# Kernel optimization log

Measured on AMD Instinct MI355X. Metric: run time of the kernel, lower is better.

The kernel has to match this reference:

```python
import jax, jax.numpy as jnp
import numpy as np

TEMPERATURE = 0.1
EPS = 1e-12  # matches F.normalize eps clamp


def setup_inputs() -> dict:
    key = jax.random.key(0)
    k1, k2 = jax.random.split(key)
    B, D = 4096, 1024
    z1 = jax.random.normal(k1, (B, D), dtype=jnp.float32)
    z2 = jax.random.normal(k2, (B, D), dtype=jnp.float32)
    return {"z1": z1, "z2": z2}


def reference(z1, z2):
    B = z1.shape[0]
    # L2-normalize rows (F.normalize dim=1, eps clamp)
    n1 = z1 / jnp.maximum(jnp.linalg.norm(z1, axis=1, keepdims=True), EPS)
    n2 = z2 / jnp.maximum(jnp.linalg.norm(z2, axis=1, keepdims=True), EPS)
    reps = jnp.concatenate([n1, n2], axis=0)  # [2B, D]
    # Rows are unit-norm, so cosine similarity == dot product -> one GEMM
    sim = (reps @ reps.T) / TEMPERATURE  # [2B, 2B]
    # positives: diag offsets +B and -B
    pos = jnp.concatenate([jnp.diagonal(sim, B), jnp.diagonal(sim, -B)])  # [2B]
    # logits row i = [pos_i, sim[i, j != i]]. logsumexp over that set =
    # logaddexp(pos_i, logsumexp over the row with the main diagonal removed).
    eye = jnp.eye(2 * B, dtype=bool)
    masked = jnp.where(eye, -jnp.inf, sim)
    lse_neg = jax.scipy.special.logsumexp(masked, axis=1)  # [2B]
    lse = jnp.logaddexp(pos, lse_neg)
    # CrossEntropyLoss with labels==0 -> mean(lse - logit_0) = mean(lse - pos)
    return jnp.mean(lse - pos)
```

## Files before the change

### kernel.cpp

```cpp
#include <hip/hip_runtime.h>

#define D_DIM 1024
#define B_HALF 4096
#define NROWS 8192
#define INV_TEMP 10.0f
#define NT 32
#define NKT 16

typedef __bf16 bf16x8 __attribute__((ext_vector_type(8)));
typedef float floatx4 __attribute__((ext_vector_type(4)));

#define MFMA16 __builtin_amdgcn_mfma_f32_16x16x32_bf16

__device__ __forceinline__ unsigned short f32_to_bf16(float f) {
    union { float f; unsigned u; } v; v.f = f;
    unsigned r = 0x7FFFu + ((v.u >> 16) & 1u);
    return (unsigned short)((v.u + r) >> 16);
}

__global__ __launch_bounds__(256) void normalize_kernel(
    const float* __restrict__ z1, const float* __restrict__ z2,
    unsigned short* __restrict__ R)
{
    const int row = blockIdx.x;
    const int tid = threadIdx.x;
    const float* src = (row < B_HALF) ? (z1 + (size_t)row * D_DIM)
                                      : (z2 + (size_t)(row - B_HALF) * D_DIM);
    float4 v = ((const float4*)src)[tid];
    float ss = v.x * v.x + v.y * v.y + v.z * v.z + v.w * v.w;
    #pragma unroll
    for (int off = 32; off > 0; off >>= 1) ss += __shfl_down(ss, off);
    __shared__ float wsum[4];
    if ((tid & 63) == 0) wsum[tid >> 6] = ss;
    __syncthreads();
    float tot = wsum[0] + wsum[1] + wsum[2] + wsum[3];
    float scale = 1.0f / fmaxf(sqrtf(tot), 1e-12f);
    ushort4 o;
    o.x = f32_to_bf16(v.x * scale);
    o.y = f32_to_bf16(v.y * scale);
    o.z = f32_to_bf16(v.z * scale);
    o.w = f32_to_bf16(v.w * scale);
    ((ushort4*)(R + (size_t)row * D_DIM))[tid] = o;
}

__global__ __launch_bounds__(512, 2) void gemm_lse_kernel(
    const unsigned short* __restrict__ R,
    float* __restrict__ partial, float* __restrict__ pos)
{
    __shared__ unsigned short lds[2][2][256 * 64];

    int t = blockIdx.x;
    int rt = 0;
    while (t >= NT - rt) { t -= NT - rt; ++rt; }
    const int ct = rt + t;
    const bool isDiag = (rt == ct);

    const int tid = threadIdx.x;
    const int wave = tid >> 6, lane = tid & 63;
    const int wm = wave >> 2, wn = wave & 3;
    const int row0 = rt * 256, col0 = ct * 256;
    const int lm = lane & 15, lq = lane >> 4;

    const unsigned short* __restrict__ gA = R + (size_t)row0 * D_DIM;
    const unsigned short* __restrict__ gB = R + (size_t)col0 * D_DIM;

    const int sRow  = lane >> 3;
    const int sSlot = (lane & 7) ^ sRow;
    const int aOff = (wm * 128 + lm) * 64;
    const int bOff = (wn * 64 + lm) * 64;
    const int sk0 = ((0 + lq) ^ (lm & 7)) * 8;
    const int sk1 = ((4 + lq) ^ (lm & 7)) * 8;

    floatx4 acc[8][4] = {};

#define STAGE_A(dstbuf, kk) \
    { _Pragma("unroll") \
      for (int i = 0; i < 4; ++i) \
        __builtin_amdgcn_global_load_lds( \
          (const __attribute__((address_space(1))) unsigned int*)(gA + (size_t)(i * 64 + wave * 8 + sRow) * D_DIM + (kk) + sSlot * 8), \
          (__attribute__((address_space(3))) unsigned int*)(&lds[dstbuf][0][(i * 64 + wave * 8) * 64]), \
          16, 0, 0); }

#define STAGE_B(dstbuf, kk) \
    { _Pragma("unroll") \
      for (int i = 0; i < 4; ++i) \
        __builtin_amdgcn_global_load_lds( \
          (const __attribute__((address_space(1))) unsigned int*)(gB + (size_t)(i * 64 + wave * 8 + sRow) * D_DIM + (kk) + sSlot * 8), \
          (__attribute__((address_space(3))) unsigned int*)(&lds[dstbuf][1][(i * 64 + wave * 8) * 64]), \
          16, 0, 0); }

    STAGE_A(0, 0)
    STAGE_B(0, 0)
    asm volatile("s_waitcnt vmcnt(0)" ::: "memory");
    __builtin_amdgcn_s_barrier();

    bf16x8 a[4][2];
    bf16x8 b[2][2][2];

    for (int kt = 0; kt < NKT; ++kt) {
        const int buf = kt & 1;
        const unsigned short* As = &lds[buf][0][0];
        const unsigned short* Bs = &lds[buf][1][0];
        const int kn = (kt + 1) * 64;
        const bool more = (kt + 1 < NKT);

        if (more) STAGE_A(buf ^ 1, kn)
        #pragma unroll
        for (int mi = 0; mi < 4; ++mi) {
            a[mi][0] = *(const bf16x8*)(As + aOff + mi * 1024 + sk0);
            a[mi][1] = *(const bf16x8*)(As + aOff + mi * 1024 + sk1);
        }
        #pragma unroll
        for (int ni = 0; ni < 2; ++ni) {
            b[0][ni][0] = *(const bf16x8*)(Bs + bOff + ni * 1024 + sk0);
            b[0][ni][1] = *(const bf16x8*)(Bs + bOff + ni * 1024 + sk1);
        }
        __builtin_amdgcn_s_barrier();
        __builtin_amdgcn_s_setprio(1);
        #pragma unroll
        for (int mi = 0; mi < 4; ++mi)
            #pragma unroll
            for (int ni = 0; ni < 2; ++ni) {
                acc[mi][ni] = MFMA16(a[mi][0], b[0][ni][0], acc[mi][ni], 0, 0, 0);
                acc[mi][ni] = MFMA16(a[mi][1], b[0][ni][1], acc[mi][ni], 0, 0, 0);
            }
        __builtin_amdgcn_s_setprio(0);
        __builtin_amdgcn_s_barrier();

        if (more) STAGE_B(buf ^ 1, kn)
        #pragma unroll
        for (int ni = 0; ni < 2; ++ni) {
            b[1][ni][0] = *(const bf16x8*)(Bs + bOff + (2 + ni) * 1024 + sk0);
            b[1][ni][1] = *(const bf16x8*)(Bs + bOff + (2 + ni) * 1024 + sk1);
        }
        __builtin_amdgcn_s_barrier();
        __builtin_amdgcn_s_setprio(1);
        #pragma unroll
        for (int mi = 0; mi < 4; ++mi)
            #pragma unroll
            for (int ni = 0; ni < 2; ++ni) {
                acc[mi][2 + ni] = MFMA16(a[mi][0], b[1][ni][0], acc[mi][2 + ni], 0, 0, 0);
                acc[mi][2 + ni] = MFMA16(a[mi][1], b[1][ni][1], acc[mi][2 + ni], 0, 0, 0);
            }
        __builtin_amdgcn_s_setprio(0);
        __builtin_amdgcn_s_barrier();

        #pragma unroll
        for (int mi = 0; mi < 4; ++mi) {
            a[mi][0] = *(const bf16x8*)(As + aOff + (4 + mi) * 1024 + sk0);
            a[mi][1] = *(const bf16x8*)(As + aOff + (4 + mi) * 1024 + sk1);
        }
        __builtin_amdgcn_s_barrier();
        __builtin_amdgcn_s_setprio(1);
        #pragma unroll
        for (int mi = 0; mi < 4; ++mi)
            #pragma unroll
            for (int ni = 0; ni < 2; ++ni) {
                acc[4 + mi][ni] = MFMA16(a[mi][0], b[0][ni][0], acc[4 + mi][ni], 0, 0, 0);
                acc[4 + mi][ni] = MFMA16(a[mi][1], b[0][ni][1], acc[4 + mi][ni], 0, 0, 0);
            }
        __builtin_amdgcn_s_setprio(0);
        __builtin_amdgcn_s_barrier();

        __builtin_amdgcn_s_setprio(1);
        #pragma unroll
        for (int mi = 0; mi < 4; ++mi)
            #pragma unroll
            for (int ni = 0; ni < 2; ++ni) {
                acc[4 + mi][2 + ni] = MFMA16(a[mi][0], b[1][ni][0], acc[4 + mi][2 + ni], 0, 0, 0);
                acc[4 + mi][2 + ni] = MFMA16(a[mi][1], b[1][ni][1], acc[4 + mi][2 + ni], 0, 0, 0);
            }
        __builtin_amdgcn_s_setprio(0);
        asm volatile("s_waitcnt vmcnt(0)" ::: "memory");
        __builtin_amdgcn_s_barrier();
        asm volatile("" ::: "memory");
    }

    float* rowsum = (float*)&lds[0][0][0];
    float* colsum = rowsum + 4 * 256;

    float ecol[4] = {0.0f, 0.0f, 0.0f, 0.0f};
    #pragma unroll
    for (int mi = 0; mi < 8; ++mi) {
        #pragma unroll
        for (int reg = 0; reg < 4; ++reg) {
            const int gr = row0 + wm * 128 + mi * 16 + lq * 4 + reg;
            float esum = 0.0f;
            #pragma unroll
            for (int ni = 0; ni < 4; ++ni) {
                const int gc = col0 + wn * 64 + ni * 16 + lm;
                float s = acc[mi][ni][reg] * INV_TEMP;
                if (gc == gr + B_HALF) { pos[gr] = s; pos[gc] = s; }
                float e = (gc == gr) ? 0.0f : __expf(s);
                esum += e;
                ecol[ni] += e;
            }
            esum += __shfl_xor(esum, 1);
            esum += __shfl_xor(esum, 2);
            esum += __shfl_xor(esum, 4);
            esum += __shfl_xor(esum, 8);
            if (lm == 0) rowsum[wn * 256 + wm * 128 + mi * 16 + lq * 4 + reg] = esum;
        }
    }
    #pragma unroll
    for (int ni = 0; ni < 4; ++ni) {
        ecol[ni] += __shfl_xor(ecol[ni], 16);
        ecol[ni] += __shfl_xor(ecol[ni], 32);
    }
    if (lq == 0 && !isDiag) {
        #pragma unroll
        for (int ni = 0; ni < 4; ++ni)
            colsum[wm * 256 + wn * 64 + ni * 16 + lm] = ecol[ni];
    }
    __syncthreads();
    if (tid < 256) {
        float rs = rowsum[0 * 256 + tid] + rowsum[1 * 256 + tid]
                 + rowsum[2 * 256 + tid] + rowsum[3 * 256 + tid];
        partial[(size_t)(row0 + tid) * NT + ct] = rs;
        if (!isDiag) {
            float cs = colsum[0 * 256 + tid] + colsum[1 * 256 + tid];
            partial[(size_t)(col0 + tid) * NT + rt] = cs;
        }
    }
}

__global__ __launch_bounds__(256) void finalize_kernel(
    const float* __restrict__ partial, const float* __restrict__ pos,
    float* __restrict__ out)
{
    const int r = blockIdx.x * 256 + threadIdx.x;
    const float4* p = (const float4*)(partial + (size_t)r * NT);
    float S = 0.0f;
    #pragma unroll
    for (int i = 0; i < 8; ++i) { float4 v = p[i]; S += (v.x + v.y) + (v.z + v.w); }
    const float po = pos[r];
    float contrib = log1pf(S * __expf(-po));
    #pragma unroll
    for (int off = 32; off > 0; off >>= 1) contrib += __shfl_down(contrib, off);
    __shared__ float wsum[4];
    if ((threadIdx.x & 63) == 0) wsum[threadIdx.x >> 6] = contrib;
    __syncthreads();
    if (threadIdx.x == 0)
        atomicAdd(out, (wsum[0] + wsum[1] + wsum[2] + wsum[3]) * (1.0f / 8192.0f));
}

extern "C" void kernel_launch(void* const* d_in, const int* in_sizes, int n_in,
                              void* d_out, int out_size, void* d_ws, size_t ws_size,
                              hipStream_t stream)
{
    const float* z1 = (const float*)d_in[0];
    const float* z2 = (const float*)d_in[1];
    float* out = (float*)d_out;
    char* ws = (char*)d_ws;
    unsigned short* R = (unsigned short*)ws;
    float* partial = (float*)(ws + (size_t)16 * 1024 * 1024);
    float* pos     = (float*)(ws + (size_t)18 * 1024 * 1024);

    hipMemsetAsync(d_out, 0, sizeof(float), stream);
    normalize_kernel<<<NROWS, 256, 0, stream>>>(z1, z2, R);
    gemm_lse_kernel<<<528, 512, 0, stream>>>(R, partial, pos);
    finalize_kernel<<<32, 256, 0, stream>>>(partial, pos, out);
}
```

Baseline: 181.9 us.

## Halve GEMM K-tile to 32 and simplify main loop to single MFMA phase

Shrinks the K tile from 64 to 32, which halves LDS per buffer and doubles the loop trip count. The four-phase interleaved loop, with its staged A/B prefetch and several barriers, becomes one phase: load all A/B fragments, issue 32 MFMAs, then wait and barrier once. The swizzle and staging layout are redone for 32-wide rows. The smaller LDS footprint could allow more resident blocks and the loop has fewer barriers, but each iteration now has less work to hide global-load latency behind.

```diff
diff --git a/kernel.cpp b/kernel.cpp
--- a/kernel.cpp
+++ b/kernel.cpp
@@ -5,7 +5,7 @@
 #define NROWS 8192
 #define INV_TEMP 10.0f
 #define NT 32
-#define NKT 16
+#define NKT 32
 
 typedef __bf16 bf16x8 __attribute__((ext_vector_type(8)));
 typedef float floatx4 __attribute__((ext_vector_type(4)));
@@ -47,7 +47,7 @@
     const unsigned short* __restrict__ R,
     float* __restrict__ partial, float* __restrict__ pos)
 {
-    __shared__ unsigned short lds[2][2][256 * 64];
+    __shared__ unsigned short lds[2][2][256 * 32];
 
     int t = blockIdx.x;
     int rt = 0;
@@ -64,116 +64,56 @@
     const unsigned short* __restrict__ gA = R + (size_t)row0 * D_DIM;
     const unsigned short* __restrict__ gB = R + (size_t)col0 * D_DIM;
 
-    const int sRow  = lane >> 3;
-    const int sSlot = (lane & 7) ^ sRow;
-    const int aOff = (wm * 128 + lm) * 64;
-    const int bOff = (wn * 64 + lm) * 64;
-    const int sk0 = ((0 + lq) ^ (lm & 7)) * 8;
-    const int sk1 = ((4 + lq) ^ (lm & 7)) * 8;
+    const int sRow = lane >> 2;
+    const int sCol = (lane & 3) ^ ((sRow >> 1) & 3);
+    const int sk = ((lq ^ ((lm >> 1) & 3)) * 8);
+    const int aBase = (wm * 128 + lm) * 32 + sk;
+    const int bBase = (wn * 64 + lm) * 32 + sk;
 
     floatx4 acc[8][4] = {};
 
-#define STAGE_A(dstbuf, kk) \
+#define STAGE(dstbuf, kk) \
     { _Pragma("unroll") \
-      for (int i = 0; i < 4; ++i) \
+      for (int i = 0; i < 2; ++i) { \
         __builtin_amdgcn_global_load_lds( \
-          (const __attribute__((address_space(1))) unsigned int*)(gA + (size_t)(i * 64 + wave * 8 + sRow) * D_DIM + (kk) + sSlot * 8), \
-          (__attribute__((address_space(3))) unsigned int*)(&lds[dstbuf][0][(i * 64 + wave * 8) * 64]), \
-          16, 0, 0); }
-
-#define STAGE_B(dstbuf, kk) \
-    { _Pragma("unroll") \
-      for (int i = 0; i < 4; ++i) \
+          (const __attribute__((address_space(1))) unsigned int*)(gA + (size_t)(wave * 32 + i * 16 + sRow) * D_DIM + (kk) + sCol * 8), \
+          (__attribute__((address_space(3))) unsigned int*)(&lds[dstbuf][0][(wave * 32 + i * 16) * 32]), \
+          16, 0, 0); \
         __builtin_amdgcn_global_load_lds( \
-          (const __attribute__((address_space(1))) unsigned int*)(gB + (size_t)(i * 64 + wave * 8 + sRow) * D_DIM + (kk) + sSlot * 8), \
-          (__attribute__((address_space(3))) unsigned int*)(&lds[dstbuf][1][(i * 64 + wave * 8) * 64]), \
-          16, 0, 0); }
-
-    STAGE_A(0, 0)
-    STAGE_B(0, 0)
+          (const __attribute__((address_space(1))) unsigned int*)(gB + (size_t)(wave * 32 + i * 16 + sRow) * D_DIM + (kk) + sCol * 8), \
+          (__attribute__((address_space(3))) unsigned int*)(&lds[dstbuf][1][(wave * 32 + i * 16) * 32]), \
+          16, 0, 0); \
+      } }
+
+    STAGE(0, 0)
     asm volatile("s_waitcnt vmcnt(0)" ::: "memory");
     __builtin_amdgcn_s_barrier();
-
-    bf16x8 a[4][2];
-    bf16x8 b[2][2][2];
 
     for (int kt = 0; kt < NKT; ++kt) {
         const int buf = kt & 1;
         const unsigned short* As = &lds[buf][0][0];
         const unsigned short* Bs = &lds[buf][1][0];
-        const int kn = (kt + 1) * 64;
-        const bool more = (kt + 1 < NKT);
-
-        if (more) STAGE_A(buf ^ 1, kn)
-        #pragma unroll
-        for (int mi = 0; mi < 4; ++mi) {
-            a[mi][0] = *(const bf16x8*)(As + aOff + mi * 1024 + sk0);
-            a[mi][1] = *(const bf16x8*)(As + aOff + mi * 1024 + sk1);
-        }
-        #pragma unroll
-        for (int ni = 0; ni < 2; ++ni) {
-            b[0][ni][0] = *(const bf16x8*)(Bs + bOff + ni * 1024 + sk0);
-            b[0][ni][1] = *(const bf16x8*)(Bs + bOff + ni * 1024 + sk1);
-        }
-        __builtin_amdgcn_s_barrier();
+
+        if (kt + 1 < NKT) STAGE(buf ^ 1, (kt + 1) * 32)
+
+        bf16x8 af[8], bf[4];
+        #pragma unroll
+        for (int mi = 0; mi < 8; ++mi)
+            af[mi] = *(const bf16x8*)(As + aBase + mi * 512);
+        #pragma unroll
+        for (int ni = 0; ni < 4; ++ni)
+            bf[ni] = *(const bf16x8*)(Bs + bBase + ni * 512);
+
         __builtin_amdgcn_s_setprio(1);
         #pragma unroll
-        for (int mi = 0; mi < 4; ++mi)
+        for (int mi = 0; mi < 8; ++mi)
             #pragma unroll
-            for (int ni = 0; ni < 2; ++ni) {
-                acc[mi][ni] = MFMA16(a[mi][0], b[0][ni][0], acc[mi][ni], 0, 0, 0);
-                acc[mi][ni] = MFMA16(a[mi][1], b[0][ni][1], acc[mi][ni], 0, 0, 0);
-            }
+            for (int ni = 0; ni < 4; ++ni)
+                acc[mi][ni] = MFMA16(af[mi], bf[ni], acc[mi][ni], 0, 0, 0);
         __builtin_amdgcn_s_setprio(0);
-        __builtin_amdgcn_s_barrier();
-
-        if (more) STAGE_B(buf ^ 1, kn)
-        #pragma unroll
-        for (int ni = 0; ni < 2; ++ni) {
-            b[1][ni][0] = *(const bf16x8*)(Bs + bOff + (2 + ni) * 1024 + sk0);
-            b[1][ni][1] = *(const bf16x8*)(Bs + bOff + (2 + ni) * 1024 + sk1);
-        }
-        __builtin_amdgcn_s_barrier();
-        __builtin_amdgcn_s_setprio(1);
-        #pragma unroll
-        for (int mi = 0; mi < 4; ++mi)
-            #pragma unroll
-            for (int ni = 0; ni < 2; ++ni) {
-                acc[mi][2 + ni] = MFMA16(a[mi][0], b[1][ni][0], acc[mi][2 + ni], 0, 0, 0);
-                acc[mi][2 + ni] = MFMA16(a[mi][1], b[1][ni][1], acc[mi][2 + ni], 0, 0, 0);
-            }
-        __builtin_amdgcn_s_setprio(0);
-        __builtin_amdgcn_s_barrier();
-
-        #pragma unroll
-        for (int mi = 0; mi < 4; ++mi) {
-            a[mi][0] = *(const bf16x8*)(As + aOff + (4 + mi) * 1024 + sk0);
-            a[mi][1] = *(const bf16x8*)(As + aOff + (4 + mi) * 1024 + sk1);
-        }
-        __builtin_amdgcn_s_barrier();
-        __builtin_amdgcn_s_setprio(1);
-        #pragma unroll
-        for (int mi = 0; mi < 4; ++mi)
-            #pragma unroll
-            for (int ni = 0; ni < 2; ++ni) {
-                acc[4 + mi][ni] = MFMA16(a[mi][0], b[0][ni][0], acc[4 + mi][ni], 0, 0, 0);
-                acc[4 + mi][ni] = MFMA16(a[mi][1], b[0][ni][1], acc[4 + mi][ni], 0, 0, 0);
-            }
-        __builtin_amdgcn_s_setprio(0);
-        __builtin_amdgcn_s_barrier();
-
-        __builtin_amdgcn_s_setprio(1);
-        #pragma unroll
-        for (int mi = 0; mi < 4; ++mi)
-            #pragma unroll
-            for (int ni = 0; ni < 2; ++ni) {
-                acc[4 + mi][2 + ni] = MFMA16(a[mi][0], b[1][ni][0], acc[4 + mi][2 + ni], 0, 0, 0);
-                acc[4 + mi][2 + ni] = MFMA16(a[mi][1], b[1][ni][1], acc[4 + mi][2 + ni], 0, 0, 0);
-            }
-        __builtin_amdgcn_s_setprio(0);
+
         asm volatile("s_waitcnt vmcnt(0)" ::: "memory");
         __builtin_amdgcn_s_barrier();
-        asm volatile("" ::: "memory");
     }
 
     float* rowsum = (float*)&lds[0][0][0];
```

Measured after the change: 186.8 us. 1.03x slower.

## Stage tiles in halves with finer vmcnt waits and swizzle block order

Applied to the files above, without the earlier changes.

Splits the A/B tile staging into four half-tile loads spread across the four MFMA phases. Each phase waits with partial vmcnt counts, so a load can overlap compute without draining everything at the end of the iteration. The per-wave fragment mapping changes to interleaved 64/32-row sub-blocks so each compute phase reads only the half that has already landed, and the epilogue index math is adjusted to match. Block IDs are also remapped (t&7)*66+(t>>3) to spread consecutive blocks across the triangle, likely for XCD/L2 locality. The cost is tighter correctness dependence on the vmcnt counts and barrier placement.

```diff
diff --git a/kernel.cpp b/kernel.cpp
--- a/kernel.cpp
+++ b/kernel.cpp
@@ -50,6 +50,7 @@
     __shared__ unsigned short lds[2][2][256 * 64];
 
     int t = blockIdx.x;
+    t = (t & 7) * 66 + (t >> 3);
     int rt = 0;
     while (t >= NT - rt) { t -= NT - rt; ++rt; }
     const int ct = rt + t;
@@ -64,38 +65,33 @@
     const unsigned short* __restrict__ gA = R + (size_t)row0 * D_DIM;
     const unsigned short* __restrict__ gB = R + (size_t)col0 * D_DIM;
 
-    const int sRow  = lane >> 3;
-    const int sSlot = (lane & 7) ^ sRow;
-    const int aOff = (wm * 128 + lm) * 64;
-    const int bOff = (wn * 64 + lm) * 64;
+    const int sR8 = lane >> 3;
+    const int sS8 = (lane & 7) ^ sR8;
     const int sk0 = ((0 + lq) ^ (lm & 7)) * 8;
     const int sk1 = ((4 + lq) ^ (lm & 7)) * 8;
+    const int aOff = (wm * 64 + lm) * 64;
+    const int bOff = (wn * 32 + lm) * 64;
 
     floatx4 acc[8][4] = {};
 
-#define STAGE_A(dstbuf, kk) \
-    { _Pragma("unroll") \
-      for (int i = 0; i < 4; ++i) \
+#define STAGE_HALF(d, m, h, kk) \
+    { _Pragma("unroll") for (int i = 0; i < 2; ++i) { \
         __builtin_amdgcn_global_load_lds( \
-          (const __attribute__((address_space(1))) unsigned int*)(gA + (size_t)(i * 64 + wave * 8 + sRow) * D_DIM + (kk) + sSlot * 8), \
-          (__attribute__((address_space(3))) unsigned int*)(&lds[dstbuf][0][(i * 64 + wave * 8) * 64]), \
-          16, 0, 0); }
-
-#define STAGE_B(dstbuf, kk) \
-    { _Pragma("unroll") \
-      for (int i = 0; i < 4; ++i) \
-        __builtin_amdgcn_global_load_lds( \
-          (const __attribute__((address_space(1))) unsigned int*)(gB + (size_t)(i * 64 + wave * 8 + sRow) * D_DIM + (kk) + sSlot * 8), \
-          (__attribute__((address_space(3))) unsigned int*)(&lds[dstbuf][1][(i * 64 + wave * 8) * 64]), \
-          16, 0, 0); }
-
-    STAGE_A(0, 0)
-    STAGE_B(0, 0)
-    asm volatile("s_waitcnt vmcnt(0)" ::: "memory");
+          (const __attribute__((address_space(1))) unsigned int*)( \
+            ((m) ? gB : gA) + (size_t)((h) * 128 + wave * 16 + i * 8 + sR8) * D_DIM + (kk) + sS8 * 8), \
+          (__attribute__((address_space(3))) unsigned int*)( \
+            &lds[d][m][((h) * 128 + wave * 16 + i * 8) * 64]), \
+          16, 0, 0); } }
+
+    STAGE_HALF(0, 0, 0, 0)
+    STAGE_HALF(0, 1, 0, 0)
+    STAGE_HALF(0, 1, 1, 0)
+    STAGE_HALF(0, 0, 1, 0)
+    asm volatile("s_waitcnt vmcnt(2)" ::: "memory");
     __builtin_amdgcn_s_barrier();
 
-    bf16x8 a[4][2];
-    bf16x8 b[2][2][2];
+    bf16x8 aF[4][2];
+    bf16x8 bF[2][2][2];
 
     for (int kt = 0; kt < NKT; ++kt) {
         const int buf = kt & 1;
@@ -104,76 +100,79 @@
         const int kn = (kt + 1) * 64;
         const bool more = (kt + 1 < NKT);
 
-        if (more) STAGE_A(buf ^ 1, kn)
         #pragma unroll
         for (int mi = 0; mi < 4; ++mi) {
-            a[mi][0] = *(const bf16x8*)(As + aOff + mi * 1024 + sk0);
-            a[mi][1] = *(const bf16x8*)(As + aOff + mi * 1024 + sk1);
+            aF[mi][0] = *(const bf16x8*)(As + aOff + mi * 1024 + sk0);
+            aF[mi][1] = *(const bf16x8*)(As + aOff + mi * 1024 + sk1);
         }
         #pragma unroll
         for (int ni = 0; ni < 2; ++ni) {
-            b[0][ni][0] = *(const bf16x8*)(Bs + bOff + ni * 1024 + sk0);
-            b[0][ni][1] = *(const bf16x8*)(Bs + bOff + ni * 1024 + sk1);
-        }
-        __builtin_amdgcn_s_barrier();
-        __builtin_amdgcn_s_setprio(1);
-        #pragma unroll
-        for (int mi = 0; mi < 4; ++mi)
-            #pragma unroll
-            for (int ni = 0; ni < 2; ++ni) {
-                acc[mi][ni] = MFMA16(a[mi][0], b[0][ni][0], acc[mi][ni], 0, 0, 0);
-                acc[mi][ni] = MFMA16(a[mi][1], b[0][ni][1], acc[mi][ni], 0, 0, 0);
-            }
-        __builtin_amdgcn_s_setprio(0);
-        __builtin_amdgcn_s_barrier();
-
-        if (more) STAGE_B(buf ^ 1, kn)
+            bF[0][ni][0] = *(const bf16x8*)(Bs + bOff + ni * 1024 + sk0);
+            bF[0][ni][1] = *(const bf16x8*)(Bs + bOff + ni * 1024 + sk1);
+        }
+        if (more) STAGE_HALF(buf ^ 1, 0, 0, kn)
+        __builtin_amdgcn_s_barrier();
+        __builtin_amdgcn_s_setprio(1);
+        #pragma unroll
+        for (int mi = 0; mi < 4; ++mi)
+            #pragma unroll
+            for (int ni = 0; ni < 2; ++ni) {
+                acc[mi][ni] = MFMA16(aF[mi][0], bF[0][ni][0], acc[mi][ni], 0, 0, 0);
+                acc[mi][ni] = MFMA16(aF[mi][1], bF[0][ni][1], acc[mi][ni], 0, 0, 0);
+            }
+        __builtin_amdgcn_s_setprio(0);
+        __builtin_amdgcn_s_barrier();
+
         #pragma unroll
         for (int ni = 0; ni < 2; ++ni) {
-            b[1][ni][0] = *(const bf16x8*)(Bs + bOff + (2 + ni) * 1024 + sk0);
-            b[1][ni][1] = *(const bf16x8*)(Bs + bOff + (2 + ni) * 1024 + sk1);
-        }
-        __builtin_amdgcn_s_barrier();
-        __builtin_amdgcn_s_setprio(1);
-        #pragma unroll
-        for (int mi = 0; mi < 4; ++mi)
-            #pragma unroll
-            for (int ni = 0; ni < 2; ++ni) {
-                acc[mi][2 + ni] = MFMA16(a[mi][0], b[1][ni][0], acc[mi][2 + ni], 0, 0, 0);
-                acc[mi][2 + ni] = MFMA16(a[mi][1], b[1][ni][1], acc[mi][2 + ni], 0, 0, 0);
-            }
-        __builtin_amdgcn_s_setprio(0);
+            bF[1][ni][0] = *(const bf16x8*)(Bs + bOff + 8192 + ni * 1024 + sk0);
+            bF[1][ni][1] = *(const bf16x8*)(Bs + bOff + 8192 + ni * 1024 + sk1);
+        }
+        if (more) STAGE_HALF(buf ^ 1, 1, 0, kn)
+        __builtin_amdgcn_s_barrier();
+        __builtin_amdgcn_s_setprio(1);
+        #pragma unroll
+        for (int mi = 0; mi < 4; ++mi)
+            #pragma unroll
+            for (int ni = 0; ni < 2; ++ni) {
+                acc[mi][2 + ni] = MFMA16(aF[mi][0], bF[1][ni][0], acc[mi][2 + ni], 0, 0, 0);
+                acc[mi][2 + ni] = MFMA16(aF[mi][1], bF[1][ni][1], acc[mi][2 + ni], 0, 0, 0);
+            }
+        __builtin_amdgcn_s_setprio(0);
+        if (more) { asm volatile("s_waitcnt vmcnt(4)" ::: "memory"); }
+        else      { asm volatile("s_waitcnt vmcnt(0)" ::: "memory"); }
         __builtin_amdgcn_s_barrier();
 
         #pragma unroll
         for (int mi = 0; mi < 4; ++mi) {
-            a[mi][0] = *(const bf16x8*)(As + aOff + (4 + mi) * 1024 + sk0);
-            a[mi][1] = *(const bf16x8*)(As + aOff + (4 + mi) * 1024 + sk1);
-        }
-        __builtin_amdgcn_s_barrier();
-        __builtin_amdgcn_s_setprio(1);
-        #pragma unroll
-        for (int mi = 0; mi < 4; ++mi)
-            #pragma unroll
-            for (int ni = 0; ni < 2; ++ni) {
-                acc[4 + mi][ni] = MFMA16(a[mi][0], b[0][ni][0], acc[4 + mi][ni], 0, 0, 0);
-                acc[4 + mi][ni] = MFMA16(a[mi][1], b[0][ni][1], acc[4 + mi][ni], 0, 0, 0);
-            }
-        __builtin_amdgcn_s_setprio(0);
-        __builtin_amdgcn_s_barrier();
-
-        __builtin_amdgcn_s_setprio(1);
-        #pragma unroll
-        for (int mi = 0; mi < 4; ++mi)
-            #pragma unroll
-            for (int ni = 0; ni < 2; ++ni) {
-                acc[4 + mi][2 + ni] = MFMA16(a[mi][0], b[1][ni][0], acc[4 + mi][2 + ni], 0, 0, 0);
-                acc[4 + mi][2 + ni] = MFMA16(a[mi][1], b[1][ni][1], acc[4 + mi][2 + ni], 0, 0, 0);
-            }
-        __builtin_amdgcn_s_setprio(0);
-        asm volatile("s_waitcnt vmcnt(0)" ::: "memory");
-        __builtin_amdgcn_s_barrier();
-        asm volatile("" ::: "memory");
+            aF[mi][0] = *(const bf16x8*)(As + aOff + 8192 + mi * 1024 + sk0);
+            aF[mi][1] = *(const bf16x8*)(As + aOff + 8192 + mi * 1024 + sk1);
+        }
+        if (more) STAGE_HALF(buf ^ 1, 1, 1, kn)
+        __builtin_amdgcn_s_barrier();
+        __builtin_amdgcn_s_setprio(1);
+        #pragma unroll
+        for (int mi = 0; mi < 4; ++mi)
+            #pragma unroll
+            for (int ni = 0; ni < 2; ++ni) {
+                acc[4 + mi][ni] = MFMA16(aF[mi][0], bF[0][ni][0], acc[4 + mi][ni], 0, 0, 0);
+                acc[4 + mi][ni] = MFMA16(aF[mi][1], bF[0][ni][1], acc[4 + mi][ni], 0, 0, 0);
+            }
+        __builtin_amdgcn_s_setprio(0);
+        __builtin_amdgcn_s_barrier();
+
+        if (more) STAGE_HALF(buf ^ 1, 0, 1, kn)
+        __builtin_amdgcn_s_setprio(1);
+        #pragma unroll
+        for (int mi = 0; mi < 4; ++mi)
+            #pragma unroll
+            for (int ni = 0; ni < 2; ++ni) {
+                acc[4 + mi][2 + ni] = MFMA16(aF[mi][0], bF[1][ni][0], acc[4 + mi][2 + ni], 0, 0, 0);
+                acc[4 + mi][2 + ni] = MFMA16(aF[mi][1], bF[1][ni][1], acc[4 + mi][2 + ni], 0, 0, 0);
+            }
+        __builtin_amdgcn_s_setprio(0);
+        asm volatile("s_waitcnt vmcnt(2)" ::: "memory");
+        __builtin_amdgcn_s_barrier();
     }
 
     float* rowsum = (float*)&lds[0][0][0];
@@ -182,13 +181,14 @@
     float ecol[4] = {0.0f, 0.0f, 0.0f, 0.0f};
     #pragma unroll
     for (int mi = 0; mi < 8; ++mi) {
+        const int rloc = (mi >> 2) * 128 + wm * 64 + (mi & 3) * 16 + lq * 4;
         #pragma unroll
         for (int reg = 0; reg < 4; ++reg) {
-            const int gr = row0 + wm * 128 + mi * 16 + lq * 4 + reg;
+            const int gr = row0 + rloc + reg;
             float esum = 0.0f;
             #pragma unroll
             for (int ni = 0; ni < 4; ++ni) {
-                const int gc = col0 + wn * 64 + ni * 16 + lm;
+                const int gc = col0 + (ni >> 1) * 128 + wn * 32 + (ni & 1) * 16 + lm;
                 float s = acc[mi][ni][reg] * INV_TEMP;
                 if (gc == gr + B_HALF) { pos[gr] = s; pos[gc] = s; }
                 float e = (gc == gr) ? 0.0f : __expf(s);
@@ -199,7 +199,7 @@
             esum += __shfl_xor(esum, 2);
             esum += __shfl_xor(esum, 4);
             esum += __shfl_xor(esum, 8);
-            if (lm == 0) rowsum[wn * 256 + wm * 128 + mi * 16 + lq * 4 + reg] = esum;
+            if (lm == 0) rowsum[wn * 256 + rloc + reg] = esum;
         }
     }
     #pragma unroll
@@ -210,7 +210,7 @@
     if (lq == 0 && !isDiag) {
         #pragma unroll
         for (int ni = 0; ni < 4; ++ni)
-            colsum[wm * 256 + wn * 64 + ni * 16 + lm] = ecol[ni];
+            colsum[wm * 256 + (ni >> 1) * 128 + wn * 32 + (ni & 1) * 16 + lm] = ecol[ni];
     }
     __syncthreads();
     if (tid < 256) {
```

Measured after the change: 180.9 us. About the same (-0.6%).
